# Optimization experiments

Hardware: AMD Instinct MI355X
Metric: run time of the kernel (lower is better)

Reference implementation:

```python
import jax, jax.numpy as jnp
import numpy as np

NUM_HEADS = 2


def setup_inputs() -> dict:
    key = jax.random.key(0)
    ks = jax.random.split(key, 8)
    B, C, H, W = 8, 256, 128, 128
    s = 1.0 / np.sqrt(C)
    return {
        "x": jax.random.normal(ks[0], (B, C, H, W), dtype=jnp.float32),
        "Wq": jax.random.normal(ks[1], (C, C), dtype=jnp.float32) * s,
        "bq": jax.random.normal(ks[2], (C,), dtype=jnp.float32) * 0.01,
        "Wk": jax.random.normal(ks[3], (C, C), dtype=jnp.float32) * s,
        "bk": jax.random.normal(ks[4], (C,), dtype=jnp.float32) * 0.01,
        "Wv": jax.random.normal(ks[5], (C, C), dtype=jnp.float32) * s,
        "bv": jax.random.normal(ks[6], (C,), dtype=jnp.float32) * 0.01,
        "gamma": jax.random.normal(ks[7], (1,), dtype=jnp.float32) * 0.1,
    }


def reference(x, Wq, bq, Wk, bk, Wv, bv, gamma):
    B, C, H, W = x.shape
    h = NUM_HEADS
    d = C // h
    n = H * W

    def proj(Wm, bm):
        # 1x1 conv == per-pixel linear over channels
        return jnp.einsum('oc,bchw->bohw', Wm, x) + bm[None, :, None, None]

    q = proj(Wq, bq).reshape(B, h, d, n)  # [B,h,d,HW]
    k = proj(Wk, bk).reshape(B, h, d, n)
    v = proj(Wv, bv).reshape(B, h, d, n)

    # attention over head_dim channels: [B,h,d,d] (faithful to the torch code)
    attn = jax.nn.softmax(jnp.einsum('bhdn,bhen->bhde', q, k), axis=-1)
    out = jnp.einsum('bhde,bhen->bhdn', attn, v).reshape(B, C, H, W)
    return gamma[0] * out + x
```

## Files before the change

kernel.cpp:

```cpp
#include <hip/hip_runtime.h>
#include <stdint.h>

#define NB 8
#define NC 256
#define NPIX 16384

typedef float f32x4 __attribute__((ext_vector_type(4)));
typedef short short8 __attribute__((ext_vector_type(8)));

#define WS_G     0
#define WS_S     524288
#define WS_U     526336
#define WS_W     528384
#define WS_WKT   530432
#define WS_WQT   595968
#define WS_MGBF  661504
#define WS_TV    923648

__device__ __forceinline__ void splitbf(float f, unsigned short& h, unsigned short& l) {
    __bf16 hb = (__bf16)f;
    float r = f - (float)hb;
    __bf16 lb = (__bf16)r;
    h = __builtin_bit_cast(unsigned short, hb);
    l = __builtin_bit_cast(unsigned short, lb);
}

__device__ __forceinline__ unsigned short bf16bits(float f) {
    return __builtin_bit_cast(unsigned short, (__bf16)f);
}

__global__ void k_misc(const float* __restrict__ Wq, const float* __restrict__ Wk,
                       float* __restrict__ WqT, float* __restrict__ WkT,
                       float* __restrict__ S) {
    int c = blockIdx.x, t = threadIdx.x;
    WqT[c * 256 + t] = Wq[t * 256 + c];
    WkT[c * 256 + t] = Wk[t * 256 + c];
    if (c < 8) S[c * 256 + t] = 0.f;
}

__global__ __launch_bounds__(512, 2) void k_gemmA(const float* __restrict__ X,
                                                  float* __restrict__ Pout,
                                                  float* __restrict__ S) {
    int bx = blockIdx.x;
    int b = bx >> 6, ch = bx & 63;
    int tid = threadIdx.x;
    int lane = tid & 63;
    int w = tid >> 6;
    int wrow = w >> 2, wcol = w & 3;
    int lrow = lane & 15;
    int lk8 = (lane >> 4) << 3;

    __shared__ __align__(16) unsigned short Thi[256 * 64];
    __shared__ __align__(16) unsigned short Tlo[256 * 64];

    f32x4 zero4 = {0.f, 0.f, 0.f, 0.f};
    f32x4 acc[8][4];
#pragma unroll
    for (int mi = 0; mi < 8; ++mi)
#pragma unroll
        for (int ni = 0; ni < 4; ++ni) acc[mi][ni] = zero4;

    float rsum[8];
#pragma unroll
    for (int i = 0; i < 8; ++i) rsum[i] = 0.f;

    const float* Xb = X + (size_t)b * NC * NPIX + ch * 256;

    for (int kk = 0; kk < 4; ++kk) {
        __syncthreads();
#pragma unroll
        for (int i = 0; i < 8; ++i) {
            int flat = tid + i * 512;
            int r = flat >> 4;
            int k4 = flat & 15;
            float4 v = *(const float4*)(Xb + (size_t)r * NPIX + kk * 64 + k4 * 4);
            rsum[i] += v.x + v.y + v.z + v.w;
            unsigned short h0, h1, h2, h3, l0, l1, l2, l3;
            splitbf(v.x, h0, l0); splitbf(v.y, h1, l1);
            splitbf(v.z, h2, l2); splitbf(v.w, h3, l3);
            int e0 = (r * 64 + k4 * 4) ^ ((r & 7) << 3);
            uint2 hu, lu;
            hu.x = (unsigned)h0 | ((unsigned)h1 << 16);
            hu.y = (unsigned)h2 | ((unsigned)h3 << 16);
            lu.x = (unsigned)l0 | ((unsigned)l1 << 16);
            lu.y = (unsigned)l2 | ((unsigned)l3 << 16);
            *(uint2*)&Thi[e0] = hu;
            *(uint2*)&Tlo[e0] = lu;
        }
        __syncthreads();
#pragma unroll
        for (int ks = 0; ks < 2; ++ks) {
            short8 bh[4], bl[4];
#pragma unroll
            for (int ni = 0; ni < 4; ++ni) {
                int row = wcol * 64 + ni * 16 + lrow;
                int e = (row * 64 + ks * 32 + lk8) ^ ((row & 7) << 3);
                bh[ni] = *(const short8*)&Thi[e];
                bl[ni] = *(const short8*)&Tlo[e];
            }
#pragma unroll
            for (int mi = 0; mi < 8; ++mi) {
                int row = wrow * 128 + mi * 16 + lrow;
                int e = (row * 64 + ks * 32 + lk8) ^ ((row & 7) << 3);
                short8 ah = *(const short8*)&Thi[e];
                short8 al = *(const short8*)&Tlo[e];
#pragma unroll
                for (int ni = 0; ni < 4; ++ni) {
                    acc[mi][ni] = __builtin_amdgcn_mfma_f32_16x16x32_bf16(ah, bh[ni], acc[mi][ni], 0, 0, 0);
                    acc[mi][ni] = __builtin_amdgcn_mfma_f32_16x16x32_bf16(ah, bl[ni], acc[mi][ni], 0, 0, 0);
                    acc[mi][ni] = __builtin_amdgcn_mfma_f32_16x16x32_bf16(al, bh[ni], acc[mi][ni], 0, 0, 0);
                }
            }
        }
    }
    float* pb = Pout + ((size_t)(b * 64 + ch)) * 65536;
    int lr4 = (lane >> 4) << 2;
    int lc = lane & 15;
#pragma unroll
    for (int mi = 0; mi < 8; ++mi)
#pragma unroll
        for (int ni = 0; ni < 4; ++ni)
#pragma unroll
            for (int j = 0; j < 4; ++j) {
                int gr = wrow * 128 + mi * 16 + lr4 + j;
                int gc = wcol * 64 + ni * 16 + lc;
                pb[gr * 256 + gc] = acc[mi][ni][j];
            }
#pragma unroll
    for (int i = 0; i < 8; ++i) {
        float rs = rsum[i];
        rs += __shfl_down(rs, 8, 16);
        rs += __shfl_down(rs, 4, 16);
        rs += __shfl_down(rs, 2, 16);
        rs += __shfl_down(rs, 1, 16);
        if ((tid & 15) == 0)
            atomicAdd(&S[b * 256 + (tid >> 4) + 32 * i], rs);
    }
}

__global__ void k_reduce(const float* __restrict__ Pin, float* __restrict__ G) {
    int bx = blockIdx.x;
    int b = bx >> 5, seg = bx & 31;
    int t = threadIdx.x;
#pragma unroll
    for (int k = 0; k < 8; ++k) {
        int i = seg * 2048 + k * 256 + t;
        float s = 0.f;
        for (int chk = 0; chk < 64; ++chk)
            s += Pin[((size_t)(b * 64 + chk)) * 65536 + i];
        G[(size_t)b * 65536 + i] = s;
    }
}

__global__ void k_uw(const float* __restrict__ WqT, const float* __restrict__ WkT,
                     const float* __restrict__ S, float* __restrict__ U,
                     float* __restrict__ Wvec) {
    int b = blockIdx.x, d = threadIdx.x;
    __shared__ float sl[256];
    sl[d] = S[b * 256 + d];
    __syncthreads();
    float u = 0.f, w = 0.f;
    for (int c = 0; c < 256; ++c) {
        float sv = sl[c];
        u += WqT[c * 256 + d] * sv;
        w += WkT[c * 256 + d] * sv;
    }
    U[b * 256 + d] = u;
    Wvec[b * 256 + d] = w;
}

__global__ __launch_bounds__(256) void k_mid(const float* __restrict__ Wq,
                                             const float* __restrict__ G,
                                             const float* __restrict__ WkT,
                                             const float* __restrict__ Wv,
                                             const float* __restrict__ bq,
                                             const float* __restrict__ bk,
                                             const float* __restrict__ bv,
                                             const float* __restrict__ U,
                                             const float* __restrict__ Wvec,
                                             const float* __restrict__ gamma,
                                             unsigned short* __restrict__ Mgb,
                                             float* __restrict__ Tvec) {
    int bx = blockIdx.x;
    int b = bx >> 4, dt = bx & 15;
    int Dbase = dt * 16;
    int h = dt >> 3;
    int t = threadIdx.x;
    int rg = t >> 5;
    int cg = t & 31;
    int r0 = rg * 2, r1 = r0 + 1;

    __shared__ __align__(16) float smem[24576];
    float* WqL = smem;
    float* PqL = smem + 4096;
    float* BIG = smem + 8192;
    float* AttL = smem;

#pragma unroll
    for (int i = 0; i < 4; ++i) {
        int f = t + i * 256;
        int row = f >> 6, c4 = (f & 63) * 4;
        *(float4*)&WqL[row * 256 + c4] = *(const float4*)(Wq + (size_t)(Dbase + row) * 256 + c4);
    }

    f32x4 pqA0 = {0,0,0,0}, pqA1 = pqA0, pqB0 = pqA0, pqB1 = pqA0;
    const float* Gb = G + (size_t)b * 65536;
    for (int p = 0; p < 4; ++p) {
        __syncthreads();
#pragma unroll
        for (int i = 0; i < 16; ++i) {
            int f = t + i * 256;
            int row = f >> 6, c4 = (f & 63) * 4;
            *(float4*)&BIG[row * 256 + c4] = *(const float4*)(Gb + (size_t)(p * 64 + row) * 256 + c4);
        }
        __syncthreads();
#pragma unroll 2
        for (int c = 0; c < 64; ++c) {
            float wq0 = WqL[r0 * 256 + p * 64 + c];
            float wq1 = WqL[r1 * 256 + p * 64 + c];
            f32x4 ga = *(const f32x4*)&BIG[c * 256 + cg * 4];
            f32x4 gb = *(const f32x4*)&BIG[c * 256 + 128 + cg * 4];
            pqA0 += wq0 * ga; pqB0 += wq0 * gb;
            pqA1 += wq1 * ga; pqB1 += wq1 * gb;
        }
    }
    __syncthreads();
    *(f32x4*)&PqL[r0 * 256 + cg * 4]       = pqA0;
    *(f32x4*)&PqL[r0 * 256 + 128 + cg * 4] = pqB0;
    *(f32x4*)&PqL[r1 * 256 + cg * 4]       = pqA1;
    *(f32x4*)&PqL[r1 * 256 + 128 + cg * 4] = pqB1;
    __syncthreads();

    f32x4 l0 = {0,0,0,0}, l1 = l0;
    for (int q = 0; q < 2; ++q) {
        if (q) __syncthreads();
#pragma unroll
        for (int i = 0; i < 16; ++i) {
            int f = t + i * 256;
            int row = f >> 5, c4 = (f & 31) * 4;
            *(float4*)&BIG[row * 128 + c4] = *(const float4*)(WkT + (size_t)(q * 128 + row) * 256 + h * 128 + c4);
        }
        __syncthreads();
#pragma unroll 2
        for (int c = 0; c < 128; ++c) {
            float p0 = PqL[r0 * 256 + q * 128 + c];
            float p1 = PqL[r1 * 256 + q * 128 + c];
            f32x4 kv = *(const f32x4*)&BIG[c * 128 + cg * 4];
            l0 += p0 * kv;
            l1 += p1 * kv;
        }
    }

    int D0 = Dbase + r0, D1 = Dbase + r1;
    float bq0 = bq[D0], bq1 = bq[D1];
    float u0 = U[b * 256 + D0], u1 = U[b * 256 + D1];
    float g0 = gamma[0];
    float m0 = -3.0e38f, m1 = -3.0e38f;
#pragma unroll
    for (int j = 0; j < 4; ++j) {
        int E = h * 128 + cg * 4 + j;
        float wv = Wvec[b * 256 + E];
        float bkE = bk[E];
        float t0 = l0[j] + bq0 * wv + bkE * u0 + 16384.f * bq0 * bkE;
        float t1 = l1[j] + bq1 * wv + bkE * u1 + 16384.f * bq1 * bkE;
        l0[j] = t0; l1[j] = t1;
        m0 = fmaxf(m0, t0); m1 = fmaxf(m1, t1);
    }
#pragma unroll
    for (int k = 1; k < 32; k <<= 1) {
        m0 = fmaxf(m0, __shfl_xor(m0, k, 32));
        m1 = fmaxf(m1, __shfl_xor(m1, k, 32));
    }
    float s0 = 0.f, s1 = 0.f;
#pragma unroll
    for (int j = 0; j < 4; ++j) {
        float e0 = __expf(l0[j] - m0);
        float e1 = __expf(l1[j] - m1);
        l0[j] = e0; l1[j] = e1;
        s0 += e0; s1 += e1;
    }
#pragma unroll
    for (int k = 1; k < 32; k <<= 1) {
        s0 += __shfl_xor(s0, k, 32);
        s1 += __shfl_xor(s1, k, 32);
    }
    float inv0 = 1.f / s0, inv1 = 1.f / s1;
    float tv0 = 0.f, tv1 = 0.f;
#pragma unroll
    for (int j = 0; j < 4; ++j) {
        float a0 = l0[j] * inv0;
        float a1 = l1[j] * inv1;
        l0[j] = a0; l1[j] = a1;
        float bvE = bv[h * 128 + cg * 4 + j];
        tv0 += a0 * bvE; tv1 += a1 * bvE;
    }
#pragma unroll
    for (int k = 1; k < 32; k <<= 1) {
        tv0 += __shfl_xor(tv0, k, 32);
        tv1 += __shfl_xor(tv1, k, 32);
    }
    __syncthreads();
    *(f32x4*)&AttL[r0 * 128 + cg * 4] = l0;
    *(f32x4*)&AttL[r1 * 128 + cg * 4] = l1;
    if (cg == 0) {
        Tvec[b * 256 + D0] = g0 * tv0;
        Tvec[b * 256 + D1] = g0 * tv1;
    }

    for (int q2 = 0; q2 < 2; ++q2) {
        __syncthreads();
#pragma unroll
        for (int i = 0; i < 16; ++i) {
            int f = t + i * 256;
            int row = f >> 5, c4 = (f & 31) * 4;
            *(float4*)&BIG[row * 128 + c4] = *(const float4*)(Wv + (size_t)(h * 128 + row) * 256 + q2 * 128 + c4);
        }
        __syncthreads();
        f32x4 mg0 = {0,0,0,0}, mg1 = mg0;
#pragma unroll 2
        for (int e = 0; e < 128; ++e) {
            float a0 = AttL[r0 * 128 + e];
            float a1 = AttL[r1 * 128 + e];
            f32x4 wv = *(const f32x4*)&BIG[e * 128 + cg * 4];
            mg0 += a0 * wv;
            mg1 += a1 * wv;
        }
        uint2 w0, w1;
        w0.x = (unsigned)bf16bits(g0 * mg0[0]) | ((unsigned)bf16bits(g0 * mg0[1]) << 16);
        w0.y = (unsigned)bf16bits(g0 * mg0[2]) | ((unsigned)bf16bits(g0 * mg0[3]) << 16);
        w1.x = (unsigned)bf16bits(g0 * mg1[0]) | ((unsigned)bf16bits(g0 * mg1[1]) << 16);
        w1.y = (unsigned)bf16bits(g0 * mg1[2]) | ((unsigned)bf16bits(g0 * mg1[3]) << 16);
        *(uint2*)(Mgb + ((size_t)(b * 256 + D0)) * 256 + q2 * 128 + cg * 4) = w0;
        *(uint2*)(Mgb + ((size_t)(b * 256 + D1)) * 256 + q2 * 128 + cg * 4) = w1;
    }
}

__global__ __launch_bounds__(256, 2) void k_gemmC(const float* __restrict__ X,
                                                  const unsigned short* __restrict__ Mgb,
                                                  const float* __restrict__ Tvec,
                                                  float* __restrict__ Y) {
    int bx = blockIdx.x;
    int b = bx >> 8, nt = bx & 255;
    int n0 = nt * 64;
    int tid = threadIdx.x;
    int lane = tid & 63, w = tid >> 6;

    __shared__ float XL[256 * 64];

    const float* Xb = X + (size_t)b * NC * NPIX + n0;
#pragma unroll
    for (int i = 0; i < 16; ++i) {
        int flat = tid + i * 256;
        int c = flat >> 4;
        int n4 = (flat & 15) * 4;
        *(float4*)&XL[c * 64 + n4] = *(const float4*)(Xb + (size_t)c * NPIX + n4);
    }
    __syncthreads();

    int lr = lane & 15;
    int lk = (lane >> 4) * 8;

    f32x4 zero4 = {0.f, 0.f, 0.f, 0.f};
    f32x4 acc[4][4];
#pragma unroll
    for (int mi = 0; mi < 4; ++mi)
#pragma unroll
        for (int ni = 0; ni < 4; ++ni) acc[mi][ni] = zero4;

    const unsigned short* Mb = Mgb + (size_t)b * 65536;
    for (int ks = 0; ks < 8; ++ks) {
        int cb = ks * 32 + lk;
        short8 afr[4];
#pragma unroll
        for (int mi = 0; mi < 4; ++mi) {
            int r = w * 64 + mi * 16 + lr;
            afr[mi] = *(const short8*)(Mb + (size_t)r * 256 + cb);
        }
        short8 bfr[4];
#pragma unroll
        for (int ni = 0; ni < 4; ++ni) {
            int nn = ni * 16 + lr;
            short8 bb;
#pragma unroll
            for (int m = 0; m < 8; ++m) {
                float xv = XL[(cb + m) * 64 + nn];
                bb[m] = (short)bf16bits(xv);
            }
            bfr[ni] = bb;
        }
#pragma unroll
        for (int mi = 0; mi < 4; ++mi)
#pragma unroll
            for (int ni = 0; ni < 4; ++ni)
                acc[mi][ni] = __builtin_amdgcn_mfma_f32_16x16x32_bf16(afr[mi], bfr[ni], acc[mi][ni], 0, 0, 0);
    }
    int lr4 = (lane >> 4) * 4;
    int lc = lane & 15;
#pragma unroll
    for (int mi = 0; mi < 4; ++mi) {
#pragma unroll
        for (int j = 0; j < 4; ++j) {
            int r = w * 64 + mi * 16 + lr4 + j;
            float tv = Tvec[b * 256 + r];
            float* yr = Y + ((size_t)(b * 256 + r)) * NPIX + n0;
#pragma unroll
            for (int ni = 0; ni < 4; ++ni) {
                int nn = ni * 16 + lc;
                yr[nn] = acc[mi][ni][j] + tv + XL[r * 64 + nn];
            }
        }
    }
}

extern "C" void kernel_launch(void* const* d_in, const int* in_sizes, int n_in,
                              void* d_out, int out_size, void* d_ws, size_t ws_size,
                              hipStream_t stream) {
    (void)in_sizes; (void)n_in; (void)out_size; (void)ws_size;
    const float* X     = (const float*)d_in[0];
    const float* Wq    = (const float*)d_in[1];
    const float* bq    = (const float*)d_in[2];
    const float* Wk    = (const float*)d_in[3];
    const float* bk    = (const float*)d_in[4];
    const float* Wv    = (const float*)d_in[5];
    const float* bv    = (const float*)d_in[6];
    const float* gamma = (const float*)d_in[7];
    float* Y  = (float*)d_out;
    float* ws = (float*)d_ws;

    float* G    = ws + WS_G;
    float* S    = ws + WS_S;
    float* U    = ws + WS_U;
    float* Wvec = ws + WS_W;
    float* WkT  = ws + WS_WKT;
    float* WqT  = ws + WS_WQT;
    unsigned short* Mgb = (unsigned short*)(ws + WS_MGBF);
    float* Tvec = ws + WS_TV;
    float* Part = Y;

    k_misc<<<dim3(256), dim3(256), 0, stream>>>(Wq, Wk, WqT, WkT, S);
    k_gemmA<<<dim3(512), dim3(512), 0, stream>>>(X, Part, S);
    k_reduce<<<dim3(256), dim3(256), 0, stream>>>(Part, G);
    k_uw<<<dim3(8), dim3(256), 0, stream>>>(WqT, WkT, S, U, Wvec);
    k_mid<<<dim3(128), dim3(256), 0, stream>>>(Wq, G, WkT, Wv, bq, bk, bv, U, Wvec, gamma, Mgb, Tvec);
    k_gemmC<<<dim3(2048), dim3(256), 0, stream>>>(X, Mgb, Tvec, Y);
}
```

Before: 419.0 us.

## Double-buffer gemmA K-loop, halve split-K partials, vectorize reduce

The Gram-matrix GEMM now gives each block twice as many pixels (512 instead of 256) and double-buffers the bf16 hi/lo LDS tiles. Global loads for the next chunk are issued before the MFMA work on the current chunk, and conversion happens afterward. With half as many partial matrices, the reduce kernel sums 32 partials using float4 vector loads instead of 64 scalar ones. LDS use doubles to 128KB per block, which may cut occupancy to one block per CU, and there are only 256 blocks.

Result: faster. 372.2 us (-11.2%).

```diff
diff --git a/kernel.cpp b/kernel.cpp
--- a/kernel.cpp
+++ b/kernel.cpp
@@ -42,7 +42,7 @@
                                                   float* __restrict__ Pout,
                                                   float* __restrict__ S) {
     int bx = blockIdx.x;
-    int b = bx >> 6, ch = bx & 63;
+    int b = bx >> 5, ch = bx & 31;
     int tid = threadIdx.x;
     int lane = tid & 63;
     int w = tid >> 6;
@@ -50,8 +50,8 @@
     int lrow = lane & 15;
     int lk8 = (lane >> 4) << 3;
 
-    __shared__ __align__(16) unsigned short Thi[256 * 64];
-    __shared__ __align__(16) unsigned short Tlo[256 * 64];
+    __shared__ __align__(16) unsigned short Thi[2][16384];
+    __shared__ __align__(16) unsigned short Tlo[2][16384];
 
     f32x4 zero4 = {0.f, 0.f, 0.f, 0.f};
     f32x4 acc[8][4];
@@ -64,29 +64,43 @@
 #pragma unroll
     for (int i = 0; i < 8; ++i) rsum[i] = 0.f;
 
-    const float* Xb = X + (size_t)b * NC * NPIX + ch * 256;
-
-    for (int kk = 0; kk < 4; ++kk) {
-        __syncthreads();
+    const float* Xb = X + (size_t)b * NC * NPIX + ch * 512;
+    int r0 = tid >> 4;
+    int k40 = tid & 15;
+
+    float4 pv[8];
+
+    auto LOAD = [&](int kk) {
+#pragma unroll
+        for (int i = 0; i < 8; ++i)
+            pv[i] = *(const float4*)(Xb + (size_t)(r0 + 32 * i) * NPIX + kk * 64 + k40 * 4);
+    };
+    auto CONV = [&](int d) {
 #pragma unroll
         for (int i = 0; i < 8; ++i) {
-            int flat = tid + i * 512;
-            int r = flat >> 4;
-            int k4 = flat & 15;
-            float4 v = *(const float4*)(Xb + (size_t)r * NPIX + kk * 64 + k4 * 4);
+            float4 v = pv[i];
             rsum[i] += v.x + v.y + v.z + v.w;
             unsigned short h0, h1, h2, h3, l0, l1, l2, l3;
             splitbf(v.x, h0, l0); splitbf(v.y, h1, l1);
             splitbf(v.z, h2, l2); splitbf(v.w, h3, l3);
-            int e0 = (r * 64 + k4 * 4) ^ ((r & 7) << 3);
+            int r = r0 + 32 * i;
+            int e0 = (r * 64 + k40 * 4) ^ ((r & 7) << 3);
             uint2 hu, lu;
             hu.x = (unsigned)h0 | ((unsigned)h1 << 16);
             hu.y = (unsigned)h2 | ((unsigned)h3 << 16);
             lu.x = (unsigned)l0 | ((unsigned)l1 << 16);
             lu.y = (unsigned)l2 | ((unsigned)l3 << 16);
-            *(uint2*)&Thi[e0] = hu;
-            *(uint2*)&Tlo[e0] = lu;
-        }
+            *(uint2*)&Thi[d][e0] = hu;
+            *(uint2*)&Tlo[d][e0] = lu;
+        }
+    };
+
+    LOAD(0);
+    CONV(0);
+
+    for (int kk = 0; kk < 8; ++kk) {
+        int cur = kk & 1;
+        if (kk < 7) LOAD(kk + 1);
         __syncthreads();
 #pragma unroll
         for (int ks = 0; ks < 2; ++ks) {
@@ -95,15 +109,15 @@
             for (int ni = 0; ni < 4; ++ni) {
                 int row = wcol * 64 + ni * 16 + lrow;
                 int e = (row * 64 + ks * 32 + lk8) ^ ((row & 7) << 3);
-                bh[ni] = *(const short8*)&Thi[e];
-                bl[ni] = *(const short8*)&Tlo[e];
+                bh[ni] = *(const short8*)&Thi[cur][e];
+                bl[ni] = *(const short8*)&Tlo[cur][e];
             }
 #pragma unroll
             for (int mi = 0; mi < 8; ++mi) {
                 int row = wrow * 128 + mi * 16 + lrow;
                 int e = (row * 64 + ks * 32 + lk8) ^ ((row & 7) << 3);
-                short8 ah = *(const short8*)&Thi[e];
-                short8 al = *(const short8*)&Tlo[e];
+                short8 ah = *(const short8*)&Thi[cur][e];
+                short8 al = *(const short8*)&Tlo[cur][e];
 #pragma unroll
                 for (int ni = 0; ni < 4; ++ni) {
                     acc[mi][ni] = __builtin_amdgcn_mfma_f32_16x16x32_bf16(ah, bh[ni], acc[mi][ni], 0, 0, 0);
@@ -112,8 +126,10 @@
                 }
             }
         }
-    }
-    float* pb = Pout + ((size_t)(b * 64 + ch)) * 65536;
+        if (kk < 7) CONV(cur ^ 1);
+    }
+
+    float* pb = Pout + ((size_t)(b * 32 + ch)) * 65536;
     int lr4 = (lane >> 4) << 2;
     int lc = lane & 15;
 #pragma unroll
@@ -134,22 +150,22 @@
         rs += __shfl_down(rs, 2, 16);
         rs += __shfl_down(rs, 1, 16);
         if ((tid & 15) == 0)
-            atomicAdd(&S[b * 256 + (tid >> 4) + 32 * i], rs);
-    }
-}
-
-__global__ void k_reduce(const float* __restrict__ Pin, float* __restrict__ G) {
+            atomicAdd(&S[b * 256 + r0 + 32 * i], rs);
+    }
+}
+
+__global__ __launch_bounds__(256) void k_reduce(const float* __restrict__ Pin,
+                                                float* __restrict__ G) {
     int bx = blockIdx.x;
-    int b = bx >> 5, seg = bx & 31;
+    int b = bx >> 6, seg = bx & 63;
     int t = threadIdx.x;
-#pragma unroll
-    for (int k = 0; k < 8; ++k) {
-        int i = seg * 2048 + k * 256 + t;
-        float s = 0.f;
-        for (int chk = 0; chk < 64; ++chk)
-            s += Pin[((size_t)(b * 64 + chk)) * 65536 + i];
-        G[(size_t)b * 65536 + i] = s;
-    }
+    size_t i0 = (size_t)seg * 1024 + (size_t)t * 4;
+    const float* base = Pin + (size_t)b * 32 * 65536 + i0;
+    f32x4 s = {0.f, 0.f, 0.f, 0.f};
+#pragma unroll 4
+    for (int chk = 0; chk < 32; ++chk)
+        s += *(const f32x4*)(base + (size_t)chk * 65536);
+    *(f32x4*)(G + (size_t)b * 65536 + i0) = s;
 }
 
 __global__ void k_uw(const float* __restrict__ WqT, const float* __restrict__ WkT,
@@ -438,8 +454,8 @@
     float* Part = Y;
 
     k_misc<<<dim3(256), dim3(256), 0, stream>>>(Wq, Wk, WqT, WkT, S);
-    k_gemmA<<<dim3(512), dim3(512), 0, stream>>>(X, Part, S);
-    k_reduce<<<dim3(256), dim3(256), 0, stream>>>(Part, G);
+    k_gemmA<<<dim3(256), dim3(512), 0, stream>>>(X, Part, S);
+    k_reduce<<<dim3(512), dim3(256), 0, stream>>>(Part, G);
     k_uw<<<dim3(8), dim3(256), 0, stream>>>(WqT, WkT, S, U, Wvec);
     k_mid<<<dim3(128), dim3(256), 0, stream>>>(Wq, G, WkT, Wv, bq, bk, bv, U, Wvec, gamma, Mgb, Tvec);
     k_gemmC<<<dim3(2048), dim3(256), 0, stream>>>(X, Mgb, Tvec, Y);
```
